# Kernel optimization log

Hardware: AMD Instinct MI355X
Metric: run time of the kernel (lower is better)

## Reference

```python
import jax, jax.numpy as jnp
import numpy as np

OUT_F, IN_F, GROUP = 4096, 4096, 64  # meta['shape'] = (OUT_F, IN_F), group_size=64, axis=1
TOKENS = 8192  # batch*seq flattened


def dequant(W_q, scale, zero):
    # unpack_4bit_u8: high nibble = first half of rows, low nibble = second half
    hi = (W_q >> 4).astype(jnp.float32)
    lo = (W_q & 0xF).astype(jnp.float32)
    W_r = jnp.concatenate([hi, lo], axis=0)      # [G, GROUP]
    W_r = (W_r - zero) * scale                   # group-wise dequant (axis=1 grouping)
    return W_r.reshape(OUT_F, IN_F)


def setup_inputs() -> dict:
    key = jax.random.key(0)
    k0, k1, k2, k3, k4 = jax.random.split(key, 5)
    G = OUT_F * IN_F // GROUP  # 262144 groups
    x = jax.random.normal(k0, (TOKENS, IN_F), dtype=jnp.float32)
    W_q = jax.random.randint(k1, (G // 2, GROUP), 0, 256, dtype=jnp.int32)  # packed bytes
    scale = jax.random.uniform(k2, (G, 1), dtype=jnp.float32) * 0.01 + 1e-4  # 1/scale from quantizer
    zero = jax.random.uniform(k3, (G, 1), dtype=jnp.float32) * 15.0
    bias = jax.random.normal(k4, (OUT_F,), dtype=jnp.float32)
    return {"x": x, "W_q": W_q, "scale": scale, "zero": zero, "bias": bias}


def reference(x, W_q, scale, zero, bias):
    # HQQMatmulNoCacheDeq.forward: out = x @ dequantize().T + bias
    W_r = dequant(W_q, scale, zero)              # [OUT_F, IN_F]
    return x @ W_r.T + bias                      # [TOKENS, OUT_F]
```

## Files before the change

### kernel.cpp

```cpp
#include <hip/hip_runtime.h>
#include <stdint.h>


typedef __attribute__((ext_vector_type(8))) _Float16 half8;
typedef __attribute__((ext_vector_type(4))) float f32x4;

#define M_DIM 8192
#define N_DIM 4096
#define K_DIM 4096

__device__ __forceinline__ void async16(const void* g, void* l) {
  __builtin_amdgcn_global_load_lds(
      (const __attribute__((address_space(1))) void*)g,
      (__attribute__((address_space(3))) void*)l,
      16, 0, 0);
}

__global__ __launch_bounds__(256) void cvt_x_f16(const float* __restrict__ x,
                                                 _Float16* __restrict__ y) {
  const size_t i = ((size_t)blockIdx.x * 256 + threadIdx.x) * 8;
  f32x4 a = *(const f32x4*)(x + i);
  f32x4 b = *(const f32x4*)(x + i + 4);
  half8 h;
  h[0] = (_Float16)a[0]; h[1] = (_Float16)a[1];
  h[2] = (_Float16)a[2]; h[3] = (_Float16)a[3];
  h[4] = (_Float16)b[0]; h[5] = (_Float16)b[1];
  h[6] = (_Float16)b[2]; h[7] = (_Float16)b[3];
  *(half8*)(y + i) = h;
}

__global__ __launch_bounds__(256) void deq_w_f16(const int* __restrict__ Wq,
                                                 const float* __restrict__ scale,
                                                 const float* __restrict__ zero,
                                                 _Float16* __restrict__ W) {
  const int idx = blockIdx.x * 256 + threadIdx.x;
  const int o  = idx >> 9;
  const int kb = (idx & 511) << 3;
  const int g  = (o << 6) + (kb >> 6);
  const int j  = kb & 63;
  const bool hi = (o < 2048);
  const int* src = Wq + (size_t)(hi ? g : g - 131072) * 64 + j;
  const int4 v0 = *(const int4*)src;
  const int4 v1 = *(const int4*)(src + 4);
  const float s  = scale[g];
  const float nz = -zero[g] * s;
  int raw[8] = {v0.x, v0.y, v0.z, v0.w, v1.x, v1.y, v1.z, v1.w};
  half8 h;
#pragma unroll
  for (int r = 0; r < 8; ++r) {
    const int nib = hi ? ((raw[r] >> 4) & 0xF) : (raw[r] & 0xF);
    h[r] = (_Float16)((float)nib * s + nz);
  }
  *(half8*)(W + (size_t)o * K_DIM + kb) = h;
}

__global__ __launch_bounds__(256) void gemm_f16_ws(const _Float16* __restrict__ A,
                                                   const _Float16* __restrict__ B,
                                                   const float* __restrict__ bias,
                                                   float* __restrict__ C) {
  __shared__ _Float16 As[128 * 32];
  __shared__ _Float16 Bs[128 * 32];

  const int tid  = threadIdx.x;
  const int wave = tid >> 6;
  const int lane = tid & 63;
  const int quad = lane >> 4;
  const int l16  = lane & 15;

  const int m0 = blockIdx.y * 128;
  const int n0 = blockIdx.x * 128;
  const int wm = (wave & 1) * 64;
  const int wn = (wave >> 1) * 64;

  const int srow = tid >> 2;
  const int scol = (tid & 3) << 3;
  const _Float16* gA0 = A + (size_t)(m0 + srow) * K_DIM + scol;
  const _Float16* gA1 = gA0 + (size_t)64 * K_DIM;
  const _Float16* gB0 = B + (size_t)(n0 + srow) * K_DIM + scol;
  const _Float16* gB1 = gB0 + (size_t)64 * K_DIM;
  _Float16* ldsA = As + wave * 512;
  _Float16* ldsB = Bs + wave * 512;

  f32x4 acc[4][4] = {};

  for (int k0 = 0; k0 < K_DIM; k0 += 32) {
    __syncthreads();
    async16(gA0 + k0, ldsA);
    async16(gA1 + k0, ldsA + 2048);
    async16(gB0 + k0, ldsB);
    async16(gB1 + k0, ldsB + 2048);
    __syncthreads();

    half8 aF[4], bF[4];
#pragma unroll
    for (int i = 0; i < 4; ++i)
      aF[i] = *(const half8*)(As + (wm + i * 16 + l16) * 32 + quad * 8);
#pragma unroll
    for (int j = 0; j < 4; ++j)
      bF[j] = *(const half8*)(Bs + (wn + j * 16 + l16) * 32 + quad * 8);
#pragma unroll
    for (int i = 0; i < 4; ++i)
#pragma unroll
      for (int j = 0; j < 4; ++j)
        acc[i][j] = __builtin_amdgcn_mfma_f32_16x16x32_f16(aF[i], bF[j],
                                                           acc[i][j], 0, 0, 0);
  }

#pragma unroll
  for (int j = 0; j < 4; ++j) {
    const int n = n0 + wn + j * 16 + l16;
    const float bv = bias[n];
#pragma unroll
    for (int i = 0; i < 4; ++i) {
      const int m = m0 + wm + i * 16 + quad * 4;
      float* p = C + (size_t)m * N_DIM + n;
      f32x4 v = acc[i][j];
      p[0 * N_DIM] = v[0] + bv;
      p[1 * N_DIM] = v[1] + bv;
      p[2 * N_DIM] = v[2] + bv;
      p[3 * N_DIM] = v[3] + bv;
    }
  }
}

__global__ __launch_bounds__(256) void gemm_fp32_fallback(
    const float* __restrict__ x, const int* __restrict__ Wq,
    const float* __restrict__ scale, const float* __restrict__ zero,
    const float* __restrict__ bias, float* __restrict__ C) {
  __shared__ float As[64][16];
  __shared__ float Bs[64][16];
  const int tid = threadIdx.x;
  const int m0 = blockIdx.y * 64;
  const int n0 = blockIdx.x * 64;
  const int tx = tid & 15;
  const int ty = tid >> 4;
  const int lr = tid >> 2;
  const int lc = (tid & 3) << 2;

  float acc[4][4] = {};

  for (int k0 = 0; k0 < K_DIM; k0 += 16) {
    __syncthreads();
    *(f32x4*)&As[lr][lc] = *(const f32x4*)(x + (size_t)(m0 + lr) * K_DIM + k0 + lc);
    {
      const int o = n0 + lr;
      const int k = k0 + lc;
      const int g = (o << 6) + (k >> 6);
      const bool hi = (o < 2048);
      const int* src = Wq + (size_t)(hi ? g : g - 131072) * 64 + (k & 63);
      const int4 v = *(const int4*)src;
      const float s = scale[g];
      const float nz = -zero[g] * s;
      f32x4 b;
      if (hi) {
        b[0] = (float)((v.x >> 4) & 0xF) * s + nz;
        b[1] = (float)((v.y >> 4) & 0xF) * s + nz;
        b[2] = (float)((v.z >> 4) & 0xF) * s + nz;
        b[3] = (float)((v.w >> 4) & 0xF) * s + nz;
      } else {
        b[0] = (float)(v.x & 0xF) * s + nz;
        b[1] = (float)(v.y & 0xF) * s + nz;
        b[2] = (float)(v.z & 0xF) * s + nz;
        b[3] = (float)(v.w & 0xF) * s + nz;
      }
      *(f32x4*)&Bs[lr][lc] = b;
    }
    __syncthreads();
#pragma unroll
    for (int kk = 0; kk < 16; ++kk) {
      float a[4], b[4];
#pragma unroll
      for (int r = 0; r < 4; ++r) a[r] = As[ty * 4 + r][kk];
#pragma unroll
      for (int c = 0; c < 4; ++c) b[c] = Bs[tx * 4 + c][kk];
#pragma unroll
      for (int r = 0; r < 4; ++r)
#pragma unroll
        for (int c = 0; c < 4; ++c) acc[r][c] += a[r] * b[c];
    }
  }
#pragma unroll
  for (int r = 0; r < 4; ++r)
#pragma unroll
    for (int c = 0; c < 4; ++c) {
      const int n = n0 + tx * 4 + c;
      C[(size_t)(m0 + ty * 4 + r) * N_DIM + n] = acc[r][c] + bias[n];
    }
}

extern "C" void kernel_launch(void* const* d_in, const int* in_sizes, int n_in,
                              void* d_out, int out_size, void* d_ws, size_t ws_size,
                              hipStream_t stream) {
  const float* x     = (const float*)d_in[0];
  const int*   Wq    = (const int*)d_in[1];
  const float* scale = (const float*)d_in[2];
  const float* zero  = (const float*)d_in[3];
  const float* bias  = (const float*)d_in[4];
  float* out = (float*)d_out;

  const size_t xh_bytes = (size_t)M_DIM * K_DIM * 2;
  const size_t wh_bytes = (size_t)N_DIM * K_DIM * 2;

  if (ws_size >= xh_bytes + wh_bytes) {
    _Float16* xh = (_Float16*)d_ws;
    _Float16* wh = (_Float16*)((char*)d_ws + xh_bytes);
    cvt_x_f16<<<M_DIM * K_DIM / (256 * 8), 256, 0, stream>>>(x, xh);
    deq_w_f16<<<N_DIM * K_DIM / (256 * 8), 256, 0, stream>>>(Wq, scale, zero, wh);
    dim3 grid(N_DIM / 128, M_DIM / 128);
    gemm_f16_ws<<<grid, 256, 0, stream>>>(xh, wh, bias, out);
  } else {
    dim3 grid(N_DIM / 64, M_DIM / 64);
    gemm_fp32_fallback<<<grid, 256, 0, stream>>>(x, Wq, scale, zero, bias, out);
  }
}
```

Measured before the change: 569.8 us.

## Double-buffer GEMM LDS with register prefetch, XOR swizzle, and fuse dequant nibble halves

```diff
diff --git a/kernel.cpp b/kernel.cpp
--- a/kernel.cpp
+++ b/kernel.cpp
@@ -8,13 +8,6 @@
 #define M_DIM 8192
 #define N_DIM 4096
 #define K_DIM 4096
-
-__device__ __forceinline__ void async16(const void* g, void* l) {
-  __builtin_amdgcn_global_load_lds(
-      (const __attribute__((address_space(1))) void*)g,
-      (__attribute__((address_space(3))) void*)l,
-      16, 0, 0);
-}
 
 __global__ __launch_bounds__(256) void cvt_x_f16(const float* __restrict__ x,
                                                  _Float16* __restrict__ y) {
@@ -36,30 +29,30 @@
   const int idx = blockIdx.x * 256 + threadIdx.x;
   const int o  = idx >> 9;
   const int kb = (idx & 511) << 3;
-  const int g  = (o << 6) + (kb >> 6);
-  const int j  = kb & 63;
-  const bool hi = (o < 2048);
-  const int* src = Wq + (size_t)(hi ? g : g - 131072) * 64 + j;
+  const int gh = (o << 6) + (kb >> 6);
+  const int gl = gh + 131072;
+  const int* src = Wq + (size_t)gh * 64 + (kb & 63);
   const int4 v0 = *(const int4*)src;
   const int4 v1 = *(const int4*)(src + 4);
-  const float s  = scale[g];
-  const float nz = -zero[g] * s;
+  const float sh = scale[gh], nzh = -zero[gh] * sh;
+  const float sl = scale[gl], nzl = -zero[gl] * sl;
   int raw[8] = {v0.x, v0.y, v0.z, v0.w, v1.x, v1.y, v1.z, v1.w};
-  half8 h;
+  half8 h, l;
 #pragma unroll
   for (int r = 0; r < 8; ++r) {
-    const int nib = hi ? ((raw[r] >> 4) & 0xF) : (raw[r] & 0xF);
-    h[r] = (_Float16)((float)nib * s + nz);
+    h[r] = (_Float16)((float)((raw[r] >> 4) & 0xF) * sh + nzh);
+    l[r] = (_Float16)((float)(raw[r] & 0xF) * sl + nzl);
   }
   *(half8*)(W + (size_t)o * K_DIM + kb) = h;
-}
-
-__global__ __launch_bounds__(256) void gemm_f16_ws(const _Float16* __restrict__ A,
-                                                   const _Float16* __restrict__ B,
-                                                   const float* __restrict__ bias,
-                                                   float* __restrict__ C) {
-  __shared__ _Float16 As[128 * 32];
-  __shared__ _Float16 Bs[128 * 32];
+  *(half8*)(W + (size_t)(o + 2048) * K_DIM + kb) = l;
+}
+
+__global__ __launch_bounds__(256, 3) void gemm_f16_ws(const _Float16* __restrict__ A,
+                                                      const _Float16* __restrict__ B,
+                                                      const float* __restrict__ bias,
+                                                      float* __restrict__ C) {
+  __shared__ _Float16 As[2][128 * 32];
+  __shared__ _Float16 Bs[2][128 * 32];
 
   const int tid  = threadIdx.x;
   const int wave = tid >> 6;
@@ -74,36 +67,76 @@
 
   const int srow = tid >> 2;
   const int scol = (tid & 3) << 3;
+  const int wcol = (((tid & 3) ^ ((tid >> 3) & 3)) << 3);
   const _Float16* gA0 = A + (size_t)(m0 + srow) * K_DIM + scol;
   const _Float16* gA1 = gA0 + (size_t)64 * K_DIM;
   const _Float16* gB0 = B + (size_t)(n0 + srow) * K_DIM + scol;
   const _Float16* gB1 = gB0 + (size_t)64 * K_DIM;
-  _Float16* ldsA = As + wave * 512;
-  _Float16* ldsB = Bs + wave * 512;
+  const int w0 = srow * 32 + wcol;
+  const int w1 = w0 + 64 * 32;
+
+  const int gf_off = ((quad ^ ((l16 >> 1) & 3)) << 3);
 
   f32x4 acc[4][4] = {};
-
-  for (int k0 = 0; k0 < K_DIM; k0 += 32) {
-    __syncthreads();
-    async16(gA0 + k0, ldsA);
-    async16(gA1 + k0, ldsA + 2048);
-    async16(gB0 + k0, ldsB);
-    async16(gB1 + k0, ldsB + 2048);
-    __syncthreads();
-
+  half8 st0[4], st1[4];
+
+  st0[0] = *(const half8*)(gA0);
+  st0[1] = *(const half8*)(gA1);
+  st0[2] = *(const half8*)(gB0);
+  st0[3] = *(const half8*)(gB1);
+  *(half8*)(&As[0][w0]) = st0[0];
+  *(half8*)(&As[0][w1]) = st0[1];
+  *(half8*)(&Bs[0][w0]) = st0[2];
+  *(half8*)(&Bs[0][w1]) = st0[3];
+  st1[0] = *(const half8*)(gA0 + 32);
+  st1[1] = *(const half8*)(gA1 + 32);
+  st1[2] = *(const half8*)(gB0 + 32);
+  st1[3] = *(const half8*)(gB1 + 32);
+  __syncthreads();
+
+  auto compute = [&](const _Float16* AS, const _Float16* BS) {
     half8 aF[4], bF[4];
 #pragma unroll
     for (int i = 0; i < 4; ++i)
-      aF[i] = *(const half8*)(As + (wm + i * 16 + l16) * 32 + quad * 8);
+      aF[i] = *(const half8*)(AS + (wm + i * 16 + l16) * 32 + gf_off);
 #pragma unroll
     for (int j = 0; j < 4; ++j)
-      bF[j] = *(const half8*)(Bs + (wn + j * 16 + l16) * 32 + quad * 8);
+      bF[j] = *(const half8*)(BS + (wn + j * 16 + l16) * 32 + gf_off);
 #pragma unroll
     for (int i = 0; i < 4; ++i)
 #pragma unroll
       for (int j = 0; j < 4; ++j)
         acc[i][j] = __builtin_amdgcn_mfma_f32_16x16x32_f16(aF[i], bF[j],
                                                            acc[i][j], 0, 0, 0);
+  };
+
+  for (int k0 = 0; k0 < K_DIM; k0 += 64) {
+    {
+      const int kp = (k0 + 64 < K_DIM) ? (k0 + 64) : 0;
+      st0[0] = *(const half8*)(gA0 + kp);
+      st0[1] = *(const half8*)(gA1 + kp);
+      st0[2] = *(const half8*)(gB0 + kp);
+      st0[3] = *(const half8*)(gB1 + kp);
+      compute(As[0], Bs[0]);
+      *(half8*)(&As[1][w0]) = st1[0];
+      *(half8*)(&As[1][w1]) = st1[1];
+      *(half8*)(&Bs[1][w0]) = st1[2];
+      *(half8*)(&Bs[1][w1]) = st1[3];
+      __syncthreads();
+    }
+    {
+      const int kp = (k0 + 96 < K_DIM) ? (k0 + 96) : 0;
+      st1[0] = *(const half8*)(gA0 + kp);
+      st1[1] = *(const half8*)(gA1 + kp);
+      st1[2] = *(const half8*)(gB0 + kp);
+      st1[3] = *(const half8*)(gB1 + kp);
+      compute(As[1], Bs[1]);
+      *(half8*)(&As[0][w0]) = st0[0];
+      *(half8*)(&As[0][w1]) = st0[1];
+      *(half8*)(&Bs[0][w0]) = st0[2];
+      *(half8*)(&Bs[0][w1]) = st0[3];
+      __syncthreads();
+    }
   }
 
 #pragma unroll
@@ -205,7 +238,7 @@
     _Float16* xh = (_Float16*)d_ws;
     _Float16* wh = (_Float16*)((char*)d_ws + xh_bytes);
     cvt_x_f16<<<M_DIM * K_DIM / (256 * 8), 256, 0, stream>>>(x, xh);
-    deq_w_f16<<<N_DIM * K_DIM / (256 * 8), 256, 0, stream>>>(Wq, scale, zero, wh);
+    deq_w_f16<<<N_DIM * K_DIM / (2 * 256 * 8), 256, 0, stream>>>(Wq, scale, zero, wh);
     dim3 grid(N_DIM / 128, M_DIM / 128);
     gemm_f16_ws<<<grid, 256, 0, stream>>>(xh, wh, bias, out);
   } else {
```

Result: no change. 570.6 us (+0.1%).
